# Optimization experiments

Hardware: AMD Instinct MI355X
Metric: run time of the kernel (lower is better)

Reference implementation:

```python
import jax, jax.numpy as jnp
import numpy as np
from jax import lax


def _viterbi_decode(logits, trans):
    """Batched Viterbi decode (tf.contrib.crf.crf_decode semantics, full lengths).
    logits: [B, T, U] unary potentials; trans: [U, U], trans[i, j] = score(i -> j).
    Returns int32 tags [B, T]."""
    logits_t = jnp.swapaxes(logits, 0, 1)  # [T, B, U]
    init_v = logits_t[0]                   # [B, U]

    def fwd_step(v, logit_t):
        # scores[b, i, j] = v[b, i] + trans[i, j]
        scores = v[:, :, None] + trans[None, :, :]          # [B, U, U]
        bp = jnp.argmax(scores, axis=1).astype(jnp.int32)   # [B, U] best prev tag
        v_new = jnp.max(scores, axis=1) + logit_t           # [B, U]
        return v_new, bp

    v_last, bps = lax.scan(fwd_step, init_v, logits_t[1:])  # bps: [T-1, B, U]
    last_tag = jnp.argmax(v_last, axis=1).astype(jnp.int32)  # [B]

    def bwd_step(tag, bp):
        # tag is the tag at t+1; bp[b, k] = best tag at t given tag k at t+1
        new_tag = jnp.take_along_axis(bp, tag[:, None], axis=1)[:, 0]
        return new_tag, new_tag

    _, tags_prefix = lax.scan(bwd_step, last_tag, bps, reverse=True)  # [T-1, B]
    tags = jnp.concatenate([tags_prefix, last_tag[None, :]], axis=0)  # [T, B]
    return jnp.swapaxes(tags, 0, 1)  # [B, T]


def setup_inputs() -> dict:
    key = jax.random.key(0)
    k0, k1, k2, k3, k4 = jax.random.split(key, 5)
    B, T, D, U = 64, 512, 1024, 128
    x = jax.random.normal(k0, (B, T, D), dtype=jnp.float32)
    kernel = jax.random.normal(k1, (D, U), dtype=jnp.float32) * (1.0 / np.sqrt(D))
    bias = jnp.zeros((U,), dtype=jnp.float32)
    chain_kernel = jax.random.normal(k2, (U, U), dtype=jnp.float32) * 0.1
    left_boundary = jax.random.normal(k3, (U,), dtype=jnp.float32) * 0.1
    right_boundary = jax.random.normal(k4, (U,), dtype=jnp.float32) * 0.1
    return {
        "x": x,
        "kernel": kernel,
        "bias": bias,
        "chain_kernel": chain_kernel,
        "left_boundary": left_boundary,
        "right_boundary": right_boundary,
    }


def reference(x, kernel, bias, chain_kernel, left_boundary, right_boundary):
    # _dense_layer: linear activation, x @ kernel + bias
    logits = jnp.einsum("btd,du->btu", x, kernel) + bias  # [B, T, U]
    # add_boundary_energy with mask=None: boundaries on first / last timestep
    logits = logits.at[:, 0, :].add(left_boundary)
    logits = logits.at[:, -1, :].add(right_boundary)
    # test_mode='viterbi', learn_mode='join': return decoded tags cast to float32
    tags = _viterbi_decode(logits, chain_kernel)
    return tags.astype(jnp.float32)
```

## Files before the change

### kernel.cpp

```cpp
#include <hip/hip_runtime.h>

#define T_SEQ 512
#define U_TAGS 128
#define D_DIM 1024
#define M_ROWS (64 * T_SEQ)

__global__ __launch_bounds__(256) void crf_gemm_half(
    const float* __restrict__ A, const float* __restrict__ Bk,
    float* __restrict__ Cpart) {
  __shared__ float As[16][132];
  __shared__ float Bs[16][132];
  const int tid = threadIdx.x;
  const int tx = tid & 15, ty = tid >> 4;
  const int row0 = blockIdx.x * 128;
  const int kbase = blockIdx.y * (D_DIM / 2);

  const int am = tid >> 2, ak = (tid & 3) << 2;
  const int bk = tid >> 5, bn = (tid & 31) << 2;

  float acc[8][8] = {};

  float4 a0 = *(const float4*)&A[(size_t)(row0 + am) * D_DIM + kbase + ak];
  float4 a1 = *(const float4*)&A[(size_t)(row0 + am + 64) * D_DIM + kbase + ak];
  float4 b0 = *(const float4*)&Bk[(size_t)(kbase + bk) * U_TAGS + bn];
  float4 b1 = *(const float4*)&Bk[(size_t)(kbase + bk + 8) * U_TAGS + bn];

  for (int k0 = 0; k0 < D_DIM / 2; k0 += 16) {
    As[ak + 0][am] = a0.x; As[ak + 1][am] = a0.y;
    As[ak + 2][am] = a0.z; As[ak + 3][am] = a0.w;
    As[ak + 0][am + 64] = a1.x; As[ak + 1][am + 64] = a1.y;
    As[ak + 2][am + 64] = a1.z; As[ak + 3][am + 64] = a1.w;
    *(float4*)&Bs[bk][bn] = b0;
    *(float4*)&Bs[bk + 8][bn] = b1;
    __syncthreads();
    if (k0 + 16 < D_DIM / 2) {
      const int kn = kbase + k0 + 16;
      a0 = *(const float4*)&A[(size_t)(row0 + am) * D_DIM + kn + ak];
      a1 = *(const float4*)&A[(size_t)(row0 + am + 64) * D_DIM + kn + ak];
      b0 = *(const float4*)&Bk[(size_t)(kn + bk) * U_TAGS + bn];
      b1 = *(const float4*)&Bk[(size_t)(kn + bk + 8) * U_TAGS + bn];
    }
#pragma unroll
    for (int kk = 0; kk < 16; ++kk) {
      float a[8], b[8];
      *(float4*)&a[0] = *(const float4*)&As[kk][ty * 8];
      *(float4*)&a[4] = *(const float4*)&As[kk][ty * 8 + 4];
      *(float4*)&b[0] = *(const float4*)&Bs[kk][tx * 4];
      *(float4*)&b[4] = *(const float4*)&Bs[kk][tx * 4 + 64];
#pragma unroll
      for (int r = 0; r < 8; ++r)
#pragma unroll
        for (int c = 0; c < 8; ++c) acc[r][c] = fmaf(a[r], b[c], acc[r][c]);
    }
    __syncthreads();
  }

  float* Cp = Cpart + (size_t)blockIdx.y * M_ROWS * U_TAGS;
#pragma unroll
  for (int r = 0; r < 8; ++r) {
    const int row = row0 + ty * 8 + r;
    *(float4*)&Cp[(size_t)row * U_TAGS + tx * 4] = *(float4*)&acc[r][0];
    *(float4*)&Cp[(size_t)row * U_TAGS + tx * 4 + 64] = *(float4*)&acc[r][4];
  }
}

__global__ __launch_bounds__(256) void crf_combine(
    float* __restrict__ p, const float* __restrict__ bias,
    const float* __restrict__ lb, const float* __restrict__ rb) {
  const int i = blockIdx.x * 256 + threadIdx.x;
  const int row = i >> 5;
  const int col = (i & 31) << 2;
  const int t = row & (T_SEQ - 1);
  const float* p1 = p + (size_t)M_ROWS * U_TAGS;
  float4 v0 = *(const float4*)&p[(size_t)i * 4];
  float4 v1 = *(const float4*)&p1[(size_t)i * 4];
  float4 bb = *(const float4*)&bias[col];
  float4 o;
  o.x = v0.x + v1.x + bb.x; o.y = v0.y + v1.y + bb.y;
  o.z = v0.z + v1.z + bb.z; o.w = v0.w + v1.w + bb.w;
  if (t == 0) {
    float4 l = *(const float4*)&lb[col];
    o.x += l.x; o.y += l.y; o.z += l.z; o.w += l.w;
  }
  if (t == T_SEQ - 1) {
    float4 r = *(const float4*)&rb[col];
    o.x += r.x; o.y += r.y; o.z += r.z; o.w += r.w;
  }
  *(float4*)&p[(size_t)i * 4] = o;
}

__global__ __launch_bounds__(256) void crf_gemm(
    const float* __restrict__ A, const float* __restrict__ Bk,
    const float* __restrict__ bias, const float* __restrict__ lb,
    const float* __restrict__ rb, float* __restrict__ C) {
  __shared__ float As[16][132];
  __shared__ float Bs[16][132];
  const int tid = threadIdx.x;
  const int tx = tid & 15, ty = tid >> 4;
  const int row0 = blockIdx.x * 128;
  const int am = tid >> 2, ak = (tid & 3) << 2;
  const int bk = tid >> 5, bn = (tid & 31) << 2;
  float acc[8][8] = {};
  float4 a0 = *(const float4*)&A[(size_t)(row0 + am) * D_DIM + ak];
  float4 a1 = *(const float4*)&A[(size_t)(row0 + am + 64) * D_DIM + ak];
  float4 b0 = *(const float4*)&Bk[(size_t)bk * U_TAGS + bn];
  float4 b1 = *(const float4*)&Bk[(size_t)(bk + 8) * U_TAGS + bn];
  for (int k0 = 0; k0 < D_DIM; k0 += 16) {
    As[ak + 0][am] = a0.x; As[ak + 1][am] = a0.y;
    As[ak + 2][am] = a0.z; As[ak + 3][am] = a0.w;
    As[ak + 0][am + 64] = a1.x; As[ak + 1][am + 64] = a1.y;
    As[ak + 2][am + 64] = a1.z; As[ak + 3][am + 64] = a1.w;
    *(float4*)&Bs[bk][bn] = b0;
    *(float4*)&Bs[bk + 8][bn] = b1;
    __syncthreads();
    if (k0 + 16 < D_DIM) {
      a0 = *(const float4*)&A[(size_t)(row0 + am) * D_DIM + k0 + 16 + ak];
      a1 = *(const float4*)&A[(size_t)(row0 + am + 64) * D_DIM + k0 + 16 + ak];
      b0 = *(const float4*)&Bk[(size_t)(k0 + 16 + bk) * U_TAGS + bn];
      b1 = *(const float4*)&Bk[(size_t)(k0 + 16 + bk + 8) * U_TAGS + bn];
    }
#pragma unroll
    for (int kk = 0; kk < 16; ++kk) {
      float a[8], b[8];
      *(float4*)&a[0] = *(const float4*)&As[kk][ty * 8];
      *(float4*)&a[4] = *(const float4*)&As[kk][ty * 8 + 4];
      *(float4*)&b[0] = *(const float4*)&Bs[kk][tx * 4];
      *(float4*)&b[4] = *(const float4*)&Bs[kk][tx * 4 + 64];
#pragma unroll
      for (int r = 0; r < 8; ++r)
#pragma unroll
        for (int c = 0; c < 8; ++c) acc[r][c] = fmaf(a[r], b[c], acc[r][c]);
    }
    __syncthreads();
  }
#pragma unroll
  for (int r = 0; r < 8; ++r) {
    const int row = row0 + ty * 8 + r;
    const int t = row & (T_SEQ - 1);
    const int n0 = tx * 4, n1 = tx * 4 + 64;
    float o[8];
#pragma unroll
    for (int c = 0; c < 4; ++c) {
      float v = acc[r][c] + bias[n0 + c];
      if (t == 0) v += lb[n0 + c];
      if (t == T_SEQ - 1) v += rb[n0 + c];
      o[c] = v;
    }
#pragma unroll
    for (int c = 0; c < 4; ++c) {
      float v = acc[r][c + 4] + bias[n1 + c];
      if (t == 0) v += lb[n1 + c];
      if (t == T_SEQ - 1) v += rb[n1 + c];
      o[c + 4] = v;
    }
    *(float4*)&C[(size_t)row * U_TAGS + n0] = *(float4*)&o[0];
    *(float4*)&C[(size_t)row * U_TAGS + n1] = *(float4*)&o[4];
  }
}

__device__ __forceinline__ void barrier_lds_only() {
  asm volatile("s_waitcnt lgkmcnt(0)\n\ts_barrier" ::: "memory");
}
__device__ __forceinline__ float fmax_dpp1(float m) {
  int i = __builtin_amdgcn_mov_dpp(__float_as_int(m), 0xB1, 0xF, 0xF, true);
  return fmaxf(m, __int_as_float(i));
}
__device__ __forceinline__ float fmax_dpp2(float m) {
  int i = __builtin_amdgcn_mov_dpp(__float_as_int(m), 0x4E, 0xF, 0xF, true);
  return fmaxf(m, __int_as_float(i));
}
__device__ __forceinline__ int imin_dpp1(int v) {
  int i = __builtin_amdgcn_mov_dpp(v, 0xB1, 0xF, 0xF, true);
  return v < i ? v : i;
}
__device__ __forceinline__ int imin_dpp2(int v) {
  int i = __builtin_amdgcn_mov_dpp(v, 0x4E, 0xF, 0xF, true);
  return v < i ? v : i;
}
__device__ __forceinline__ float max3f(float a, float b, float c) {
  return fmaxf(fmaxf(a, b), c);
}

__global__ __launch_bounds__(512) void crf_viterbi(
    const float* __restrict__ logits,
    const float* __restrict__ trans,
    float* __restrict__ out) {
  __shared__ __align__(16) float vbuf[2][4][136];
  __shared__ __align__(16) unsigned char bp[T_SEQ * U_TAGS];
  __shared__ unsigned char tags[T_SEQ];
  __shared__ unsigned char M[8][U_TAGS];
  __shared__ int seedL[8];
  __shared__ float red_v[8];
  __shared__ int red_i[8];

  const int b = blockIdx.x;
  const int tid = threadIdx.x;
  const int j = tid >> 2;
  const int seg = tid & 3;
  const float* lg_b = logits + (size_t)b * T_SEQ * U_TAGS;

  float* tstage = (float*)bp;
#pragma unroll
  for (int it = 0; it < 8; ++it)
    *(float4*)&tstage[(it * 512 + tid) * 4] =
        *(const float4*)&trans[(it * 512 + tid) * 4];
  __syncthreads();
  float tr[32];
#pragma unroll
  for (int e = 0; e < 32; ++e) tr[e] = tstage[(seg * 32 + e) * U_TAGS + j];
  if (tid < U_TAGS) {
    float v0 = lg_b[tid];
#pragma unroll
    for (int cp = 0; cp < 4; ++cp) vbuf[0][cp][tid] = v0;
  }
  __syncthreads();

  float lgp0 = lg_b[1 * U_TAGS + j];
  float lgp1 = lg_b[2 * U_TAGS + j];
  for (int t = 1; t < T_SEQ; ++t) {
    int tp = t + 2; if (tp > T_SEQ - 1) tp = T_SEQ - 1;
    float lgnew = lg_b[(size_t)tp * U_TAGS + j];

    const float* vrow = &vbuf[(t - 1) & 1][seg][seg * 32];
    float s[32];
#pragma unroll
    for (int q = 0; q < 8; ++q) {
      float4 vv = *(const float4*)&vrow[q * 4];
      s[q * 4 + 0] = vv.x + tr[q * 4 + 0];
      s[q * 4 + 1] = vv.y + tr[q * 4 + 1];
      s[q * 4 + 2] = vv.z + tr[q * 4 + 2];
      s[q * 4 + 3] = vv.w + tr[q * 4 + 3];
    }
    float a0 = max3f(s[0], s[1], s[2]),   a1 = max3f(s[3], s[4], s[5]);
    float a2 = max3f(s[6], s[7], s[8]),   a3 = max3f(s[9], s[10], s[11]);
    float a4 = max3f(s[12], s[13], s[14]), a5 = max3f(s[15], s[16], s[17]);
    float a6 = max3f(s[18], s[19], s[20]), a7 = max3f(s[21], s[22], s[23]);
    float a8 = max3f(s[24], s[25], s[26]), a9 = max3f(s[27], s[28], s[29]);
    float a10 = fmaxf(s[30], s[31]);
    float b0 = max3f(a0, a1, a2), b1 = max3f(a3, a4, a5);
    float b2 = max3f(a6, a7, a8), b3 = fmaxf(a9, a10);
    float m = fmaxf(max3f(b0, b1, b2), b3);
    m = fmax_dpp1(m);
    m = fmax_dpp2(m);
    int e0 = 127, e1 = 127, e2 = 127, e3 = 127;
#pragma unroll
    for (int e = 7; e >= 0; --e) {
      e0 = (s[e] == m) ? e : e0;
      e1 = (s[8 + e] == m) ? 8 + e : e1;
      e2 = (s[16 + e] == m) ? 16 + e : e2;
      e3 = (s[24 + e] == m) ? 24 + e : e3;
    }
    int el = min(min(e0, e1), min(e2, e3));
    int ic = (el < 127) ? seg * 32 + el : 1023;
    ic = imin_dpp1(ic);
    ic = imin_dpp2(ic);
    if (seg == 0) {
      float vn = m + lgp0;
#pragma unroll
      for (int cp = 0; cp < 4; ++cp) vbuf[t & 1][cp][j] = vn;
      bp[(t - 1) * U_TAGS + j] = (unsigned char)ic;
    }
    lgp0 = lgp1;
    lgp1 = lgnew;
    barrier_lds_only();
  }

  if (tid < U_TAGS) {
    float val = vbuf[1][0][tid];
    int idx = tid;
#pragma unroll
    for (int off = 1; off < 64; off <<= 1) {
      float vo = __shfl_xor(val, off);
      int io = __shfl_xor(idx, off);
      if (vo > val || (vo == val && io < idx)) { val = vo; idx = io; }
    }
    if ((tid & 63) == 0) { red_v[tid >> 6] = val; red_i[tid >> 6] = idx; }
  }
  __syncthreads();
  if (tid == 0) {
    int tg = (red_v[1] > red_v[0]) ? red_i[1] : red_i[0];
    tags[T_SEQ - 1] = (unsigned char)tg;
  }
  __syncthreads();

  const int w = tid >> 6, l = tid & 63;
  const int lo = w * 64;
  const int hi = (w == 7) ? (T_SEQ - 2) : (w * 64 + 63);
  {
    int c0 = l, c1 = l + 64;
    for (int t = hi; t >= lo; --t) {
      c0 = bp[t * U_TAGS + c0];
      c1 = bp[t * U_TAGS + c1];
    }
    M[w][l] = (unsigned char)c0;
    M[w][l + 64] = (unsigned char)c1;
  }
  __syncthreads();
  if (tid == 0) {
    int sd = tags[T_SEQ - 1];
    seedL[7] = sd;
    for (int w2 = 7; w2 >= 1; --w2) { sd = M[w2][sd]; seedL[w2 - 1] = sd; }
  }
  __syncthreads();
  if (l == 0) {
    int cur = seedL[w];
    for (int t = hi; t >= lo; --t) {
      cur = bp[t * U_TAGS + cur];
      tags[t] = (unsigned char)cur;
    }
  }
  __syncthreads();
  out[(size_t)b * T_SEQ + tid] = (float)tags[tid];
}

extern "C" void kernel_launch(void* const* d_in, const int* in_sizes, int n_in,
                              void* d_out, int out_size, void* d_ws,
                              size_t ws_size, hipStream_t stream) {
  const float* x = (const float*)d_in[0];
  const float* kern = (const float*)d_in[1];
  const float* bias = (const float*)d_in[2];
  const float* chain = (const float*)d_in[3];
  const float* lb = (const float*)d_in[4];
  const float* rb = (const float*)d_in[5];
  float* out = (float*)d_out;
  float* logits = (float*)d_ws;

  const size_t part = (size_t)M_ROWS * U_TAGS * sizeof(float);
  if (ws_size >= 2 * part) {
    crf_gemm_half<<<dim3(256, 2), 256, 0, stream>>>(x, kern, logits);
    crf_combine<<<(M_ROWS * U_TAGS / 4 + 255) / 256, 256, 0, stream>>>(
        logits, bias, lb, rb);
  } else {
    crf_gemm<<<256, 256, 0, stream>>>(x, kern, bias, lb, rb, logits);
  }
  crf_viterbi<<<64, 512, 0, stream>>>(logits, chain, out);
}
```

Measured before the change: 591.4 us.

## Prune Viterbi candidates with transition bounds and split GEMM K four ways

The Viterbi forward pass now runs in a single wave with no block barriers. It uses a bound, rowmax(trans) - globalmin(trans), to keep only previous tags that could still win, via a ballot mask, and evaluates just those candidates with readlane. The GEMM split-K goes from 2 to 4 partitions when the workspace allows, to raise parallelism, and the combine kernel sums a variable number of partials. The risks are data-dependent candidate counts, extra workspace traffic from writing and re-reading four partials, and tie-breaking that must still match argmax semantics.

After: 671.7 us. 13.6% more time.

```diff
diff --git a/kernel.cpp b/kernel.cpp
--- a/kernel.cpp
+++ b/kernel.cpp
@@ -5,15 +5,15 @@
 #define D_DIM 1024
 #define M_ROWS (64 * T_SEQ)
 
-__global__ __launch_bounds__(256) void crf_gemm_half(
+__global__ __launch_bounds__(256, 4) void crf_gemm_part(
     const float* __restrict__ A, const float* __restrict__ Bk,
-    float* __restrict__ Cpart) {
+    float* __restrict__ Cpart, int kdepth) {
   __shared__ float As[16][132];
   __shared__ float Bs[16][132];
   const int tid = threadIdx.x;
   const int tx = tid & 15, ty = tid >> 4;
   const int row0 = blockIdx.x * 128;
-  const int kbase = blockIdx.y * (D_DIM / 2);
+  const int kbase = blockIdx.y * kdepth;
 
   const int am = tid >> 2, ak = (tid & 3) << 2;
   const int bk = tid >> 5, bn = (tid & 31) << 2;
@@ -25,7 +25,7 @@
   float4 b0 = *(const float4*)&Bk[(size_t)(kbase + bk) * U_TAGS + bn];
   float4 b1 = *(const float4*)&Bk[(size_t)(kbase + bk + 8) * U_TAGS + bn];
 
-  for (int k0 = 0; k0 < D_DIM / 2; k0 += 16) {
+  for (int k0 = 0; k0 < kdepth; k0 += 16) {
     As[ak + 0][am] = a0.x; As[ak + 1][am] = a0.y;
     As[ak + 2][am] = a0.z; As[ak + 3][am] = a0.w;
     As[ak + 0][am + 64] = a1.x; As[ak + 1][am + 64] = a1.y;
@@ -33,7 +33,7 @@
     *(float4*)&Bs[bk][bn] = b0;
     *(float4*)&Bs[bk + 8][bn] = b1;
     __syncthreads();
-    if (k0 + 16 < D_DIM / 2) {
+    if (k0 + 16 < kdepth) {
       const int kn = kbase + k0 + 16;
       a0 = *(const float4*)&A[(size_t)(row0 + am) * D_DIM + kn + ak];
       a1 = *(const float4*)&A[(size_t)(row0 + am + 64) * D_DIM + kn + ak];
@@ -66,18 +66,19 @@
 
 __global__ __launch_bounds__(256) void crf_combine(
     float* __restrict__ p, const float* __restrict__ bias,
-    const float* __restrict__ lb, const float* __restrict__ rb) {
+    const float* __restrict__ lb, const float* __restrict__ rb, int nparts) {
   const int i = blockIdx.x * 256 + threadIdx.x;
   const int row = i >> 5;
   const int col = (i & 31) << 2;
   const int t = row & (T_SEQ - 1);
-  const float* p1 = p + (size_t)M_ROWS * U_TAGS;
-  float4 v0 = *(const float4*)&p[(size_t)i * 4];
-  float4 v1 = *(const float4*)&p1[(size_t)i * 4];
+  float4 o = *(const float4*)&p[(size_t)i * 4];
+  for (int q = 1; q < nparts; ++q) {
+    const float* pq = p + (size_t)q * M_ROWS * U_TAGS;
+    float4 v = *(const float4*)&pq[(size_t)i * 4];
+    o.x += v.x; o.y += v.y; o.z += v.z; o.w += v.w;
+  }
   float4 bb = *(const float4*)&bias[col];
-  float4 o;
-  o.x = v0.x + v1.x + bb.x; o.y = v0.y + v1.y + bb.y;
-  o.z = v0.z + v1.z + bb.z; o.w = v0.w + v1.w + bb.w;
+  o.x += bb.x; o.y += bb.y; o.z += bb.z; o.w += bb.w;
   if (t == 0) {
     float4 l = *(const float4*)&lb[col];
     o.x += l.x; o.y += l.y; o.z += l.z; o.w += l.w;
@@ -158,152 +159,186 @@
   }
 }
 
-__device__ __forceinline__ void barrier_lds_only() {
-  asm volatile("s_waitcnt lgkmcnt(0)\n\ts_barrier" ::: "memory");
-}
-__device__ __forceinline__ float fmax_dpp1(float m) {
-  int i = __builtin_amdgcn_mov_dpp(__float_as_int(m), 0xB1, 0xF, 0xF, true);
-  return fmaxf(m, __int_as_float(i));
-}
-__device__ __forceinline__ float fmax_dpp2(float m) {
-  int i = __builtin_amdgcn_mov_dpp(__float_as_int(m), 0x4E, 0xF, 0xF, true);
-  return fmaxf(m, __int_as_float(i));
-}
-__device__ __forceinline__ int imin_dpp1(int v) {
-  int i = __builtin_amdgcn_mov_dpp(v, 0xB1, 0xF, 0xF, true);
-  return v < i ? v : i;
-}
-__device__ __forceinline__ int imin_dpp2(int v) {
-  int i = __builtin_amdgcn_mov_dpp(v, 0x4E, 0xF, 0xF, true);
-  return v < i ? v : i;
-}
-__device__ __forceinline__ float max3f(float a, float b, float c) {
-  return fmaxf(fmaxf(a, b), c);
-}
-
-__global__ __launch_bounds__(512) void crf_viterbi(
+__device__ __forceinline__ float rl_f(float v, int lane) {
+  return __int_as_float(__builtin_amdgcn_readlane(__float_as_int(v), lane));
+}
+template <int CTRL>
+__device__ __forceinline__ float dpp_max_step(float x) {
+  int v = __float_as_int(x);
+  int t = __builtin_amdgcn_update_dpp(v, v, CTRL, 0xF, 0xF, false);
+  return fmaxf(x, __int_as_float(t));
+}
+__device__ __forceinline__ float wave_max64_bcast(float x) {
+  x = dpp_max_step<0x111>(x);
+  x = dpp_max_step<0x112>(x);
+  x = dpp_max_step<0x114>(x);
+  x = dpp_max_step<0x118>(x);
+  x = dpp_max_step<0x142>(x);
+  x = dpp_max_step<0x143>(x);
+  return rl_f(x, 63);
+}
+
+__global__ __launch_bounds__(256) void crf_viterbi(
     const float* __restrict__ logits,
     const float* __restrict__ trans,
     float* __restrict__ out) {
-  __shared__ __align__(16) float vbuf[2][4][136];
-  __shared__ __align__(16) unsigned char bp[T_SEQ * U_TAGS];
+  __shared__ __align__(16) float trs[U_TAGS * U_TAGS];
+  __shared__ __align__(16) unsigned char bp[(T_SEQ - 1) * U_TAGS];
   __shared__ unsigned char tags[T_SEQ];
   __shared__ unsigned char M[8][U_TAGS];
-  __shared__ int seedL[8];
-  __shared__ float red_v[8];
-  __shared__ int red_i[8];
+  __shared__ float rmaxs[U_TAGS];
+  __shared__ float wmin2[2];
+  __shared__ float gminS;
+  __shared__ int lastTagS;
 
   const int b = blockIdx.x;
   const int tid = threadIdx.x;
-  const int j = tid >> 2;
-  const int seg = tid & 3;
   const float* lg_b = logits + (size_t)b * T_SEQ * U_TAGS;
 
-  float* tstage = (float*)bp;
-#pragma unroll
-  for (int it = 0; it < 8; ++it)
-    *(float4*)&tstage[(it * 512 + tid) * 4] =
-        *(const float4*)&trans[(it * 512 + tid) * 4];
-  __syncthreads();
-  float tr[32];
-#pragma unroll
-  for (int e = 0; e < 32; ++e) tr[e] = tstage[(seg * 32 + e) * U_TAGS + j];
+#pragma unroll
+  for (int it = 0; it < 16; ++it)
+    *(float4*)&trs[(it * 256 + tid) * 4] =
+        *(const float4*)&trans[(it * 256 + tid) * 4];
+  __syncthreads();
+
+  float rowmin = 1e30f;
   if (tid < U_TAGS) {
-    float v0 = lg_b[tid];
-#pragma unroll
-    for (int cp = 0; cp < 4; ++cp) vbuf[0][cp][tid] = v0;
-  }
-  __syncthreads();
-
-  float lgp0 = lg_b[1 * U_TAGS + j];
-  float lgp1 = lg_b[2 * U_TAGS + j];
-  for (int t = 1; t < T_SEQ; ++t) {
-    int tp = t + 2; if (tp > T_SEQ - 1) tp = T_SEQ - 1;
-    float lgnew = lg_b[(size_t)tp * U_TAGS + j];
-
-    const float* vrow = &vbuf[(t - 1) & 1][seg][seg * 32];
-    float s[32];
-#pragma unroll
-    for (int q = 0; q < 8; ++q) {
-      float4 vv = *(const float4*)&vrow[q * 4];
-      s[q * 4 + 0] = vv.x + tr[q * 4 + 0];
-      s[q * 4 + 1] = vv.y + tr[q * 4 + 1];
-      s[q * 4 + 2] = vv.z + tr[q * 4 + 2];
-      s[q * 4 + 3] = vv.w + tr[q * 4 + 3];
-    }
-    float a0 = max3f(s[0], s[1], s[2]),   a1 = max3f(s[3], s[4], s[5]);
-    float a2 = max3f(s[6], s[7], s[8]),   a3 = max3f(s[9], s[10], s[11]);
-    float a4 = max3f(s[12], s[13], s[14]), a5 = max3f(s[15], s[16], s[17]);
-    float a6 = max3f(s[18], s[19], s[20]), a7 = max3f(s[21], s[22], s[23]);
-    float a8 = max3f(s[24], s[25], s[26]), a9 = max3f(s[27], s[28], s[29]);
-    float a10 = fmaxf(s[30], s[31]);
-    float b0 = max3f(a0, a1, a2), b1 = max3f(a3, a4, a5);
-    float b2 = max3f(a6, a7, a8), b3 = fmaxf(a9, a10);
-    float m = fmaxf(max3f(b0, b1, b2), b3);
-    m = fmax_dpp1(m);
-    m = fmax_dpp2(m);
-    int e0 = 127, e1 = 127, e2 = 127, e3 = 127;
-#pragma unroll
-    for (int e = 7; e >= 0; --e) {
-      e0 = (s[e] == m) ? e : e0;
-      e1 = (s[8 + e] == m) ? 8 + e : e1;
-      e2 = (s[16 + e] == m) ? 16 + e : e2;
-      e3 = (s[24 + e] == m) ? 24 + e : e3;
-    }
-    int el = min(min(e0, e1), min(e2, e3));
-    int ic = (el < 127) ? seg * 32 + el : 1023;
-    ic = imin_dpp1(ic);
-    ic = imin_dpp2(ic);
-    if (seg == 0) {
-      float vn = m + lgp0;
-#pragma unroll
-      for (int cp = 0; cp < 4; ++cp) vbuf[t & 1][cp][j] = vn;
-      bp[(t - 1) * U_TAGS + j] = (unsigned char)ic;
-    }
-    lgp0 = lgp1;
-    lgp1 = lgnew;
-    barrier_lds_only();
-  }
-
+    float mx = -1e30f, mn = 1e30f;
+    for (int q = 0; q < 32; ++q) {
+      float4 v = *(const float4*)&trs[tid * U_TAGS + q * 4];
+      mx = fmaxf(fmaxf(mx, v.x), fmaxf(v.y, fmaxf(v.z, v.w)));
+      mn = fminf(fminf(mn, v.x), fminf(v.y, fminf(v.z, v.w)));
+    }
+    rmaxs[tid] = mx;
+    rowmin = mn;
+  }
   if (tid < U_TAGS) {
-    float val = vbuf[1][0][tid];
-    int idx = tid;
+#pragma unroll
+    for (int off = 1; off < 64; off <<= 1)
+      rowmin = fminf(rowmin, __shfl_xor(rowmin, off));
+    if ((tid & 63) == 0) wmin2[tid >> 6] = rowmin;
+  }
+  __syncthreads();
+  if (tid == 0) gminS = fminf(wmin2[0], wmin2[1]);
+  __syncthreads();
+
+  if (tid < 64) {
+    const int l = tid;
+    float v0 = lg_b[l];
+    float v1 = lg_b[64 + l];
+    const float gmin = gminS;
+    const float c0 = rmaxs[l] - gmin + 0.01f;
+    const float c1 = rmaxs[64 + l] - gmin + 0.01f;
+    float lgA0 = lg_b[U_TAGS + l], lgA1 = lg_b[U_TAGS + 64 + l];
+    float lgB0 = lg_b[2 * U_TAGS + l], lgB1 = lg_b[2 * U_TAGS + 64 + l];
+
+    for (int t = 1; t < T_SEQ; ++t) {
+      int tp = t + 2; if (tp > T_SEQ - 1) tp = T_SEQ - 1;
+      float lgC0 = lg_b[(size_t)tp * U_TAGS + l];
+      float lgC1 = lg_b[(size_t)tp * U_TAGS + 64 + l];
+
+      const float vm = wave_max64_bcast(fmaxf(v0, v1));
+      unsigned long long m0 = __ballot(v0 + c0 >= vm);
+      unsigned long long m1 = __ballot(v1 + c1 >= vm);
+
+      int a0 = -1, a1 = -1, b0 = -1, b1 = -1;
+      if (m0) { a0 = __builtin_ctzll(m0); m0 &= m0 - 1;
+        if (m0) { a1 = __builtin_ctzll(m0); m0 &= m0 - 1; } }
+      if (m1) { b0 = __builtin_ctzll(m1); m1 &= m1 - 1;
+        if (m1) { b1 = __builtin_ctzll(m1); m1 &= m1 - 1; } }
+
+      float tA00 = 0, tA01 = 0, tA10 = 0, tA11 = 0;
+      float tB00 = 0, tB01 = 0, tB10 = 0, tB11 = 0;
+      if (a0 >= 0) { tA00 = trs[a0 * U_TAGS + l]; tA01 = trs[a0 * U_TAGS + 64 + l]; }
+      if (a1 >= 0) { tA10 = trs[a1 * U_TAGS + l]; tA11 = trs[a1 * U_TAGS + 64 + l]; }
+      if (b0 >= 0) { tB00 = trs[(64 + b0) * U_TAGS + l]; tB01 = trs[(64 + b0) * U_TAGS + 64 + l]; }
+      if (b1 >= 0) { tB10 = trs[(64 + b1) * U_TAGS + l]; tB11 = trs[(64 + b1) * U_TAGS + 64 + l]; }
+
+      float best0 = -1e30f, best1 = -1e30f;
+      int bi0 = 0, bi1 = 0;
+      if (a0 >= 0) {
+        float vi = rl_f(v0, a0);
+        float s0 = vi + tA00, s1 = vi + tA01;
+        if (s0 > best0) { best0 = s0; bi0 = a0; }
+        if (s1 > best1) { best1 = s1; bi1 = a0; }
+      }
+      if (a1 >= 0) {
+        float vi = rl_f(v0, a1);
+        float s0 = vi + tA10, s1 = vi + tA11;
+        if (s0 > best0) { best0 = s0; bi0 = a1; }
+        if (s1 > best1) { best1 = s1; bi1 = a1; }
+      }
+      while (m0) {
+        int i = __builtin_ctzll(m0); m0 &= m0 - 1;
+        float vi = rl_f(v0, i);
+        float s0 = vi + trs[i * U_TAGS + l], s1 = vi + trs[i * U_TAGS + 64 + l];
+        if (s0 > best0) { best0 = s0; bi0 = i; }
+        if (s1 > best1) { best1 = s1; bi1 = i; }
+      }
+      if (b0 >= 0) {
+        float vi = rl_f(v1, b0);
+        float s0 = vi + tB00, s1 = vi + tB01;
+        if (s0 > best0) { best0 = s0; bi0 = 64 + b0; }
+        if (s1 > best1) { best1 = s1; bi1 = 64 + b0; }
+      }
+      if (b1 >= 0) {
+        float vi = rl_f(v1, b1);
+        float s0 = vi + tB10, s1 = vi + tB11;
+        if (s0 > best0) { best0 = s0; bi0 = 64 + b1; }
+        if (s1 > best1) { best1 = s1; bi1 = 64 + b1; }
+      }
+      while (m1) {
+        int i = __builtin_ctzll(m1); m1 &= m1 - 1;
+        float vi = rl_f(v1, i);
+        float s0 = vi + trs[(64 + i) * U_TAGS + l];
+        float s1 = vi + trs[(64 + i) * U_TAGS + 64 + l];
+        if (s0 > best0) { best0 = s0; bi0 = 64 + i; }
+        if (s1 > best1) { best1 = s1; bi1 = 64 + i; }
+      }
+
+      bp[(t - 1) * U_TAGS + l] = (unsigned char)bi0;
+      bp[(t - 1) * U_TAGS + 64 + l] = (unsigned char)bi1;
+      v0 = best0 + lgA0;
+      v1 = best1 + lgA1;
+      lgA0 = lgB0; lgA1 = lgB1;
+      lgB0 = lgC0; lgB1 = lgC1;
+    }
+
+    float val = v0; int idx = l;
+    if (v1 > v0) { val = v1; idx = 64 + l; }
 #pragma unroll
     for (int off = 1; off < 64; off <<= 1) {
       float vo = __shfl_xor(val, off);
       int io = __shfl_xor(idx, off);
       if (vo > val || (vo == val && io < idx)) { val = vo; idx = io; }
     }
-    if ((tid & 63) == 0) { red_v[tid >> 6] = val; red_i[tid >> 6] = idx; }
-  }
-  __syncthreads();
+    if (l == 0) { lastTagS = idx; tags[T_SEQ - 1] = (unsigned char)idx; }
+  }
+  __syncthreads();
+
+#pragma unroll
+  for (int q = 0; q < 4; ++q) {
+    const int chain = tid + q * 256;
+    const int c = chain >> 7, s = chain & 127;
+    const int lo = c * 64;
+    const int hi = (c == 7) ? (T_SEQ - 2) : (c * 64 + 63);
+    int cur = s;
+    for (int t = hi; t >= lo; --t) cur = bp[t * U_TAGS + cur];
+    M[c][s] = (unsigned char)cur;
+  }
+  __syncthreads();
+  __shared__ unsigned char seedE[8];
   if (tid == 0) {
-    int tg = (red_v[1] > red_v[0]) ? red_i[1] : red_i[0];
-    tags[T_SEQ - 1] = (unsigned char)tg;
-  }
-  __syncthreads();
-
-  const int w = tid >> 6, l = tid & 63;
-  const int lo = w * 64;
-  const int hi = (w == 7) ? (T_SEQ - 2) : (w * 64 + 63);
-  {
-    int c0 = l, c1 = l + 64;
-    for (int t = hi; t >= lo; --t) {
-      c0 = bp[t * U_TAGS + c0];
-      c1 = bp[t * U_TAGS + c1];
-    }
-    M[w][l] = (unsigned char)c0;
-    M[w][l + 64] = (unsigned char)c1;
-  }
-  __syncthreads();
-  if (tid == 0) {
-    int sd = tags[T_SEQ - 1];
-    seedL[7] = sd;
-    for (int w2 = 7; w2 >= 1; --w2) { sd = M[w2][sd]; seedL[w2 - 1] = sd; }
-  }
-  __syncthreads();
-  if (l == 0) {
-    int cur = seedL[w];
+    int e = lastTagS;
+    seedE[7] = (unsigned char)e;
+    for (int c = 7; c >= 1; --c) { e = M[c][e]; seedE[c - 1] = (unsigned char)e; }
+  }
+  __syncthreads();
+  if (tid < 8) {
+    const int c = tid;
+    const int lo = c * 64;
+    const int hi = (c == 7) ? (T_SEQ - 2) : (c * 64 + 63);
+    int cur = seedE[c];
     for (int t = hi; t >= lo; --t) {
       cur = bp[t * U_TAGS + cur];
       tags[t] = (unsigned char)cur;
@@ -311,6 +346,7 @@
   }
   __syncthreads();
   out[(size_t)b * T_SEQ + tid] = (float)tags[tid];
+  out[(size_t)b * T_SEQ + 256 + tid] = (float)tags[256 + tid];
 }
 
 extern "C" void kernel_launch(void* const* d_in, const int* in_sizes, int n_in,
@@ -326,12 +362,15 @@
   float* logits = (float*)d_ws;
 
   const size_t part = (size_t)M_ROWS * U_TAGS * sizeof(float);
-  if (ws_size >= 2 * part) {
-    crf_gemm_half<<<dim3(256, 2), 256, 0, stream>>>(x, kern, logits);
-    crf_combine<<<(M_ROWS * U_TAGS / 4 + 255) / 256, 256, 0, stream>>>(
-        logits, bias, lb, rb);
+  const int nblk = M_ROWS * U_TAGS / 4 / 256;
+  if (ws_size >= 4 * part) {
+    crf_gemm_part<<<dim3(256, 4), 256, 0, stream>>>(x, kern, logits, D_DIM / 4);
+    crf_combine<<<nblk, 256, 0, stream>>>(logits, bias, lb, rb, 4);
+  } else if (ws_size >= 2 * part) {
+    crf_gemm_part<<<dim3(256, 2), 256, 0, stream>>>(x, kern, logits, D_DIM / 2);
+    crf_combine<<<nblk, 256, 0, stream>>>(logits, bias, lb, rb, 2);
   } else {
     crf_gemm<<<256, 256, 0, stream>>>(x, kern, bias, lb, rb, logits);
   }
-  crf_viterbi<<<64, 512, 0, stream>>>(logits, chain, out);
-}
+  crf_viterbi<<<64, 256, 0, stream>>>(logits, chain, out);
+}
```
